# Performance work log

Hardware: AMD Instinct MI355X
Metric: run time of the kernel (lower is better)

The kernel has to match this reference:

```python
import jax, jax.numpy as jnp
import numpy as np

B, S, D, H, DH = 2, 2048, 1024, 16, 64  # batch, seq, d_hidden, n_head, d_head


def setup_inputs() -> dict:
    key = jax.random.key(0)
    ks = jax.random.split(key, 11)
    sc = 0.02
    inp = {
        "Q": jax.random.normal(ks[0], (B, S, D), jnp.float32),
        "K": jax.random.normal(ks[1], (B, S, D), jnp.float32),
        "V": jax.random.normal(ks[2], (B, S, D), jnp.float32),
        # causal mask: True = masked (strictly upper triangular), broadcast to [B,S,S]
        "attn_mask": jnp.broadcast_to(jnp.triu(jnp.ones((S, S), bool), k=1), (B, S, S)),
        "W_q": jax.random.normal(ks[3], (H * DH, D), jnp.float32) * sc,
        "b_q": jnp.zeros((H * DH,), jnp.float32),
        "W_k": jax.random.normal(ks[4], (H * DH, D), jnp.float32) * sc,
        "b_k": jnp.zeros((H * DH,), jnp.float32),
        "W_v": jax.random.normal(ks[5], (H * DH, D), jnp.float32) * sc,
        "b_v": jnp.zeros((H * DH,), jnp.float32),
        "W_o": jax.random.normal(ks[6], (D, H * DH), jnp.float32) * sc,
        "b_o": jnp.zeros((D,), jnp.float32),
    }
    return inp


def reference(Q, K, V, attn_mask, W_q, b_q, W_k, b_k, W_v, b_v, W_o, b_o):
    scaler = 1.0 / (DH ** 0.5)
    # projections: torch Linear is x @ W.T + b
    def proj(x, W, b):
        y = jnp.einsum('bsd,ed->bse', x, W) + b  # e = H*DH
        return y.reshape(x.shape[0], x.shape[1], H, DH).transpose(0, 2, 1, 3)  # [B,H,S,DH]
    q = proj(Q, W_q, b_q)
    k = proj(K, W_k, b_k)
    v = proj(V, W_v, b_v)
    score = jnp.einsum('bhqd,bhkd->bhqk', q, k) * scaler
    score = jnp.where(attn_mask[:, None, :, :], jnp.float32(-1e9), score)
    attn_prob = jax.nn.softmax(score, axis=-1)  # dropout p=0.0 -> identity
    context = jnp.einsum('bhqk,bhkd->bhqd', attn_prob, v)
    context = context.transpose(0, 2, 1, 3).reshape(Q.shape[0], -1, H * DH)
    output = jnp.einsum('bse,de->bsd', context, W_o) + b_o
    return (output, attn_prob)
```

## Files before the change

### kernel.cpp

```cpp
#include <hip/hip_runtime.h>
#include <hip/hip_bf16.h>

typedef __attribute__((ext_vector_type(8))) __bf16 bf16x8;
typedef __attribute__((ext_vector_type(4))) float f32x4;
typedef __attribute__((ext_vector_type(4))) float f4;

#define MB 2
#define MS 2048
#define MD 1024
#define MH 16
#define MDH 64

__device__ __forceinline__ void gl_lds16(const __bf16* g, __bf16* l) {
  __builtin_amdgcn_global_load_lds(
      (const __attribute__((address_space(1))) unsigned int*)g,
      (__attribute__((address_space(3))) unsigned int*)l, 16, 0, 0);
}

__device__ __forceinline__ void stage64(const __bf16* __restrict__ g, int gstride,
                                        __bf16* lds, int t) {
#pragma unroll
  for (int j = 0; j < 2; j++) {
    const int slot = t + j * 256;
    const int r = slot >> 3;
    const int c = (slot & 7) ^ (r & 7);
    gl_lds16(g + (size_t)r * gstride + c * 8, &lds[slot * 8]);
  }
}

__device__ __forceinline__ bf16x8 frag_ld(const __bf16* lds, int row, int kc) {
  const int slot = row * 8 + (kc ^ (row & 7));
  return *(const bf16x8*)&lds[slot * 8];
}

__global__ __launch_bounds__(256) void convert_kernel(
    const float* __restrict__ Q, const float* __restrict__ K, const float* __restrict__ V,
    const float* __restrict__ Wq, const float* __restrict__ Wk, const float* __restrict__ Wv,
    const float* __restrict__ Wo, __bf16* __restrict__ Ab, __bf16* __restrict__ Wb) {
  const size_t base = ((size_t)blockIdx.x * 256 + threadIdx.x) * 8;
  const float* src;
  __bf16* dst;
  size_t off;
  if (base < 3UL * 4194304UL) {
    const int z = (int)(base >> 22);
    off = base & 4194303UL;
    src = (z == 0) ? Q : ((z == 1) ? K : V);
    dst = Ab + ((size_t)z << 22);
  } else {
    const size_t b2 = base - 3UL * 4194304UL;
    const int w = (int)(b2 >> 20);
    off = b2 & 1048575UL;
    src = (w == 0) ? Wq : ((w == 1) ? Wk : ((w == 2) ? Wv : Wo));
    dst = Wb + ((size_t)w << 20);
  }
  f4 a = *(const f4*)(src + off);
  f4 b = *(const f4*)(src + off + 4);
  bf16x8 o;
#pragma unroll
  for (int j = 0; j < 4; j++) {
    o[j] = (__bf16)a[j];
    o[j + 4] = (__bf16)b[j];
  }
  *(bf16x8*)(dst + off) = o;
}

__device__ __forceinline__ void gemm_core(const __bf16* __restrict__ A,
                                          const __bf16* __restrict__ W,
                                          int tile_m, int tile_n,
                                          f32x4 acc[4][4]) {
  __shared__ __bf16 a_lds[8192];
  __shared__ __bf16 w_lds[8192];
  const int t = threadIdx.x;
  const int lane = t & 63, wave = t >> 6;
  const int l15 = lane & 15, quad = lane >> 4;
  const int wr = wave >> 1, wc = wave & 1;

  const f32x4 fzero = {0.f, 0.f, 0.f, 0.f};
#pragma unroll
  for (int mi = 0; mi < 4; mi++)
#pragma unroll
    for (int ni = 0; ni < 4; ni++) acc[mi][ni] = fzero;

  const __bf16* Abase = A + (size_t)(tile_m * 128) * 1024;
  const __bf16* Wbase = W + (size_t)(tile_n * 128) * 1024;

  for (int k0 = 0; k0 < 1024; k0 += 64) {
    __syncthreads();
#pragma unroll
    for (int j = 0; j < 4; j++) {
      const int slot = t + j * 256;
      const int r = slot >> 3;
      const int c = (slot & 7) ^ (r & 7);
      gl_lds16(Abase + (size_t)r * 1024 + k0 + c * 8, &a_lds[slot * 8]);
    }
#pragma unroll
    for (int j = 0; j < 4; j++) {
      const int slot = t + j * 256;
      const int r = slot >> 3;
      const int c = (slot & 7) ^ (r & 7);
      gl_lds16(Wbase + (size_t)r * 1024 + k0 + c * 8, &w_lds[slot * 8]);
    }
    __syncthreads();

#pragma unroll
    for (int kk = 0; kk < 2; kk++) {
      bf16x8 af[4], bf[4];
#pragma unroll
      for (int mi = 0; mi < 4; mi++)
        af[mi] = frag_ld(a_lds, wr * 64 + mi * 16 + l15, kk * 4 + quad);
#pragma unroll
      for (int ni = 0; ni < 4; ni++)
        bf[ni] = frag_ld(w_lds, wc * 64 + ni * 16 + l15, kk * 4 + quad);
#pragma unroll
      for (int mi = 0; mi < 4; mi++)
#pragma unroll
        for (int ni = 0; ni < 4; ni++)
          acc[mi][ni] = __builtin_amdgcn_mfma_f32_16x16x32_bf16(af[mi], bf[ni], acc[mi][ni], 0, 0, 0);
    }
  }
}

__global__ __launch_bounds__(256) void qkv_proj(
    const __bf16* __restrict__ Ab, const __bf16* __restrict__ Wb,
    const float* __restrict__ bq, const float* __restrict__ bk, const float* __restrict__ bv,
    __bf16* __restrict__ qo, __bf16* __restrict__ ko, __bf16* __restrict__ vo) {
  const int z = blockIdx.z;
  const __bf16* A = Ab + ((size_t)z << 22);
  const __bf16* W = Wb + ((size_t)z << 20);
  const float* bias = (z == 0) ? bq : ((z == 1) ? bk : bv);
  __bf16* out = (z == 0) ? qo : ((z == 1) ? ko : vo);

  f32x4 acc[4][4];
  gemm_core(A, W, blockIdx.y, blockIdx.x, acc);

  const int t = threadIdx.x;
  const int lane = t & 63, wave = t >> 6;
  const int l15 = lane & 15, quad = lane >> 4;
  const int wr = wave >> 1, wc = wave & 1;
  const float scale = (z == 0) ? 0.125f : 1.0f;

#pragma unroll
  for (int ni = 0; ni < 4; ni++) {
    const int e = blockIdx.x * 128 + wc * 64 + ni * 16 + l15;
    const float bias_v = bias[e];
    const int h = e >> 6, dh = e & 63;
#pragma unroll
    for (int mi = 0; mi < 4; mi++) {
#pragma unroll
      for (int r = 0; r < 4; r++) {
        const int sg = blockIdx.y * 128 + wr * 64 + mi * 16 + quad * 4 + r;
        const int bb = sg >> 11, s = sg & 2047;
        const float val = (acc[mi][ni][r] + bias_v) * scale;
        size_t addr;
        if (z < 2) addr = ((size_t)((bb * 16 + h) * 2048 + s)) * 64 + dh;
        else       addr = ((size_t)((bb * 16 + h) * 64 + dh)) * 2048 + s;
        out[addr] = (__bf16)val;
      }
    }
  }
}

__device__ __forceinline__ void qk_tile(const __bf16* kl, const bf16x8 qf0, const bf16x8 qf1,
                                        int l15, int quad, f32x4 sc[4]) {
  const f32x4 fzero = {0.f, 0.f, 0.f, 0.f};
#pragma unroll
  for (int blk = 0; blk < 4; blk++) {
    bf16x8 kf0 = frag_ld(kl, blk * 16 + l15, quad);
    bf16x8 kf1 = frag_ld(kl, blk * 16 + l15, 4 + quad);
    f32x4 z = fzero;
    z = __builtin_amdgcn_mfma_f32_16x16x32_bf16(qf0, kf0, z, 0, 0, 0);
    z = __builtin_amdgcn_mfma_f32_16x16x32_bf16(qf1, kf1, z, 0, 0, 0);
    sc[blk] = z;
  }
}

__device__ __forceinline__ void sm_update(const f32x4 sc[4], int kt, int q0, int wave,
                                          int quad, int l15, float m[4], float l[4]) {
#pragma unroll
  for (int r = 0; r < 4; r++) {
    const int qrow = q0 + wave * 16 + quad * 4 + r;
    float sv[4];
    float nm = m[r];
#pragma unroll
    for (int blk = 0; blk < 4; blk++) {
      const int kcol = kt * 64 + blk * 16 + l15;
      float s = sc[blk][r];
      s = (kcol > qrow) ? -1e30f : s;
      sv[blk] = s;
      nm = fmaxf(nm, s);
    }
    float acc = l[r] * __expf(m[r] - nm);
#pragma unroll
    for (int blk = 0; blk < 4; blk++) acc += __expf(sv[blk] - nm);
    l[r] = acc;
    m[r] = nm;
  }
}

__global__ __launch_bounds__(256) void attn_kernel(
    const __bf16* __restrict__ q, const __bf16* __restrict__ k,
    const __bf16* __restrict__ vt, float* __restrict__ P, __bf16* __restrict__ ctx) {
  const int qt = 31 - blockIdx.x;
  const int h = blockIdx.y, b = blockIdx.z;
  const int bh = b * 16 + h;
  const int t = threadIdx.x;
  const int lane = t & 63, wave = t >> 6;
  const int l15 = lane & 15, quad = lane >> 4;
  const int q0 = qt * 64;

  __shared__ __bf16 q_lds[4096];
  __shared__ __bf16 k_lds[4096];
  __shared__ __bf16 v_lds[4096];
  __shared__ __bf16 p_lds[4 * 16 * 72];

  const __bf16* qbase = q + ((size_t)bh * 2048 + q0) * 64;
  const __bf16* kbase = k + (size_t)bh * 2048 * 64;
  const __bf16* vbase = vt + (size_t)bh * 64 * 2048;
  float* Pbase = P + ((size_t)bh * 2048 + q0) * 2048;

  stage64(qbase, 64, q_lds, t);
  __syncthreads();
  const bf16x8 qf0 = frag_ld(q_lds, wave * 16 + l15, quad);
  const bf16x8 qf1 = frag_ld(q_lds, wave * 16 + l15, 4 + quad);

  float m[4], l[4];
#pragma unroll
  for (int r = 0; r < 4; r++) { m[r] = -1e30f; l[r] = 0.f; }

  for (int kt0 = 0; kt0 <= qt; kt0 += 2) {
    const bool two = (kt0 + 1 <= qt);
    __syncthreads();
    stage64(kbase + (size_t)kt0 * 4096, 64, k_lds, t);
    if (two) stage64(kbase + (size_t)(kt0 + 1) * 4096, 64, v_lds, t);
    __syncthreads();
    f32x4 sc[4];
    qk_tile(k_lds, qf0, qf1, l15, quad, sc);
    sm_update(sc, kt0, q0, wave, quad, l15, m, l);
    if (two) {
      qk_tile(v_lds, qf0, qf1, l15, quad, sc);
      sm_update(sc, kt0 + 1, q0, wave, quad, l15, m, l);
    }
  }

  float rl[4];
#pragma unroll
  for (int r = 0; r < 4; r++) {
    float mm = m[r], ll = l[r];
#pragma unroll
    for (int msk = 1; msk < 16; msk <<= 1) {
      const float mo = __shfl_xor(mm, msk, 64);
      const float lo = __shfl_xor(ll, msk, 64);
      const float mn = fmaxf(mm, mo);
      ll = ll * __expf(mm - mn) + lo * __expf(mo - mn);
      mm = mn;
    }
    m[r] = mm;
    rl[r] = 1.0f / ll;
  }

  const f32x4 fzero = {0.f, 0.f, 0.f, 0.f};
  f32x4 o[4];
#pragma unroll
  for (int d = 0; d < 4; d++) o[d] = fzero;

  for (int kt = 0; kt <= qt; kt++) {
    __syncthreads();
    stage64(kbase + (size_t)kt * 4096, 64, k_lds, t);
    stage64(vbase + (size_t)kt * 64, 2048, v_lds, t);
    __syncthreads();

    f32x4 sc[4];
    qk_tile(k_lds, qf0, qf1, l15, quad, sc);

#pragma unroll
    for (int r = 0; r < 4; r++) {
      const int qrow = q0 + wave * 16 + quad * 4 + r;
#pragma unroll
      for (int blk = 0; blk < 4; blk++) {
        const int kcol = kt * 64 + blk * 16 + l15;
        float s = sc[blk][r];
        s = (kcol > qrow) ? -1e30f : s;
        const float p = __expf(s - m[r]) * rl[r];
        Pbase[(size_t)(wave * 16 + quad * 4 + r) * 2048 + kcol] = p;
        p_lds[(wave * 16 + quad * 4 + r) * 72 + blk * 16 + l15] = (__bf16)p;
      }
    }
    const bf16x8 pf0 = *(const bf16x8*)&p_lds[(wave * 16 + l15) * 72 + quad * 8];
    const bf16x8 pf1 = *(const bf16x8*)&p_lds[(wave * 16 + l15) * 72 + 32 + quad * 8];
#pragma unroll
    for (int d = 0; d < 4; d++) {
      bf16x8 vf0 = frag_ld(v_lds, d * 16 + l15, quad);
      bf16x8 vf1 = frag_ld(v_lds, d * 16 + l15, 4 + quad);
      o[d] = __builtin_amdgcn_mfma_f32_16x16x32_bf16(pf0, vf0, o[d], 0, 0, 0);
      o[d] = __builtin_amdgcn_mfma_f32_16x16x32_bf16(pf1, vf1, o[d], 0, 0, 0);
    }
  }

  const int c0 = (qt + 1) * 64;
  const int zr = t >> 2;
  for (int c = c0 + (t & 3) * 4; c < 2048; c += 16)
    *(f32x4*)&Pbase[(size_t)zr * 2048 + c] = fzero;

#pragma unroll
  for (int d = 0; d < 4; d++) {
#pragma unroll
    for (int r = 0; r < 4; r++) {
      const int sl = wave * 16 + quad * 4 + r;
      const size_t idx = ((size_t)(b * 2048 + q0 + sl)) * 1024 + h * 64 + d * 16 + l15;
      ctx[idx] = (__bf16)o[d][r];
    }
  }
}

__global__ __launch_bounds__(256) void out_proj(
    const __bf16* __restrict__ ctxp, const __bf16* __restrict__ Wob,
    const float* __restrict__ bo, float* __restrict__ out) {
  f32x4 acc[4][4];
  gemm_core(ctxp, Wob, blockIdx.y, blockIdx.x, acc);

  const int t = threadIdx.x;
  const int lane = t & 63, wave = t >> 6;
  const int l15 = lane & 15, quad = lane >> 4;
  const int wr = wave >> 1, wc = wave & 1;

#pragma unroll
  for (int ni = 0; ni < 4; ni++) {
    const int e = blockIdx.x * 128 + wc * 64 + ni * 16 + l15;
    const float bias_v = bo[e];
#pragma unroll
    for (int mi = 0; mi < 4; mi++) {
#pragma unroll
      for (int r = 0; r < 4; r++) {
        const int sg = blockIdx.y * 128 + wr * 64 + mi * 16 + quad * 4 + r;
        out[(size_t)sg * 1024 + e] = acc[mi][ni][r] + bias_v;
      }
    }
  }
}

extern "C" void kernel_launch(void* const* d_in, const int* in_sizes, int n_in,
                              void* d_out, int out_size, void* d_ws, size_t ws_size,
                              hipStream_t stream) {
  const float* Q  = (const float*)d_in[0];
  const float* K  = (const float*)d_in[1];
  const float* V  = (const float*)d_in[2];
  const float* Wq = (const float*)d_in[4];
  const float* bq = (const float*)d_in[5];
  const float* Wk = (const float*)d_in[6];
  const float* bk = (const float*)d_in[7];
  const float* Wv = (const float*)d_in[8];
  const float* bv = (const float*)d_in[9];
  const float* Wo = (const float*)d_in[10];
  const float* bo = (const float*)d_in[11];

  float* out0 = (float*)d_out;
  float* P = out0 + (size_t)MB * MS * MD;

  __bf16* Ab  = (__bf16*)d_ws;
  __bf16* Wb  = Ab + 3UL * 4194304UL;
  __bf16* qws = Wb + 4UL * 1048576UL;
  __bf16* kws = qws + 4194304UL;
  __bf16* vws = kws + 4194304UL;
  __bf16* cws = vws + 4194304UL;

  convert_kernel<<<dim3(8192), 256, 0, stream>>>(Q, K, V, Wq, Wk, Wv, Wo, Ab, Wb);
  qkv_proj<<<dim3(8, 32, 3), 256, 0, stream>>>(Ab, Wb, bq, bk, bv, qws, kws, vws);
  attn_kernel<<<dim3(32, 16, 2), 256, 0, stream>>>(qws, kws, vws, P, cws);
  out_proj<<<dim3(8, 32, 1), 256, 0, stream>>>(cws, Wb + 3UL * 1048576UL, bo, out0);
}
```

Before: 772.4 us.

## Double-buffer K/V staging, swizzle P LDS, remap blocks, and specialize diagonal masking

Both attention passes now prefetch the next K (and V) tiles into alternate LDS buffers while computing on the current ones. This cuts one barrier per iteration and overlaps global-to-LDS loads with MFMA work. The P staging buffer uses an XOR swizzle in place of padding to avoid bank conflicts. Causal masking is applied only on the diagonal tile. Blocks are remapped so consecutive blocks span different heads at the same q-tile, and s_setprio raises priority around the MFMA sections. The cost is more LDS (5 tiles) and more complex indexing.

```diff
diff --git a/kernel.cpp b/kernel.cpp
--- a/kernel.cpp
+++ b/kernel.cpp
@@ -175,7 +175,8 @@
 }
 
 __device__ __forceinline__ void sm_update(const f32x4 sc[4], int kt, int q0, int wave,
-                                          int quad, int l15, float m[4], float l[4]) {
+                                          int quad, int l15, float m[4], float l[4],
+                                          bool diag) {
 #pragma unroll
   for (int r = 0; r < 4; r++) {
     const int qrow = q0 + wave * 16 + quad * 4 + r;
@@ -185,7 +186,7 @@
     for (int blk = 0; blk < 4; blk++) {
       const int kcol = kt * 64 + blk * 16 + l15;
       float s = sc[blk][r];
-      s = (kcol > qrow) ? -1e30f : s;
+      if (diag) s = (kcol > qrow) ? -1e30f : s;
       sv[blk] = s;
       nm = fmaxf(nm, s);
     }
@@ -197,49 +198,83 @@
   }
 }
 
+__device__ __forceinline__ void p_emit(const f32x4 sc[4], bool diag, int kt, int q0,
+                                       int wave, int quad, int l15,
+                                       const float m[4], const float rl[4],
+                                       float* __restrict__ Pbase, __bf16* p_lds) {
+#pragma unroll
+  for (int r = 0; r < 4; r++) {
+    const int rr = quad * 4 + r;
+    const int qrow = q0 + wave * 16 + rr;
+#pragma unroll
+    for (int blk = 0; blk < 4; blk++) {
+      const int kcol = kt * 64 + blk * 16 + l15;
+      float s = sc[blk][r];
+      if (diag) s = (kcol > qrow) ? -1e30f : s;
+      const float p = __expf(s - m[r]) * rl[r];
+      Pbase[(size_t)(wave * 16 + rr) * 2048 + kcol] = p;
+      const int cc = blk * 16 + l15;
+      const int sch = (cc >> 3) ^ (rr & 7);
+      p_lds[wave * 1024 + rr * 64 + sch * 8 + (cc & 7)] = (__bf16)p;
+    }
+  }
+}
+
 __global__ __launch_bounds__(256) void attn_kernel(
     const __bf16* __restrict__ q, const __bf16* __restrict__ k,
     const __bf16* __restrict__ vt, float* __restrict__ P, __bf16* __restrict__ ctx) {
-  const int qt = 31 - blockIdx.x;
-  const int h = blockIdx.y, b = blockIdx.z;
-  const int bh = b * 16 + h;
+  const int lin = blockIdx.x + 32 * (blockIdx.y + 16 * blockIdx.z);
+  const int x8 = lin & 7, j = lin >> 3;
+  const int bh = x8 + 8 * (j & 3);
+  const int qt = 31 - (j >> 2);
+  const int b = bh >> 4, h = bh & 15;
   const int t = threadIdx.x;
   const int lane = t & 63, wave = t >> 6;
   const int l15 = lane & 15, quad = lane >> 4;
   const int q0 = qt * 64;
 
-  __shared__ __bf16 q_lds[4096];
-  __shared__ __bf16 k_lds[4096];
-  __shared__ __bf16 v_lds[4096];
-  __shared__ __bf16 p_lds[4 * 16 * 72];
+  __shared__ __bf16 sbuf[4][4096];
+  __shared__ __bf16 p_lds[4096];
 
   const __bf16* qbase = q + ((size_t)bh * 2048 + q0) * 64;
   const __bf16* kbase = k + (size_t)bh * 2048 * 64;
   const __bf16* vbase = vt + (size_t)bh * 64 * 2048;
   float* Pbase = P + ((size_t)bh * 2048 + q0) * 2048;
 
-  stage64(qbase, 64, q_lds, t);
+  stage64(qbase, 64, sbuf[0], t);
   __syncthreads();
-  const bf16x8 qf0 = frag_ld(q_lds, wave * 16 + l15, quad);
-  const bf16x8 qf1 = frag_ld(q_lds, wave * 16 + l15, 4 + quad);
+  const bf16x8 qf0 = frag_ld(sbuf[0], wave * 16 + l15, quad);
+  const bf16x8 qf1 = frag_ld(sbuf[0], wave * 16 + l15, 4 + quad);
+  __syncthreads();
 
   float m[4], l[4];
 #pragma unroll
   for (int r = 0; r < 4; r++) { m[r] = -1e30f; l[r] = 0.f; }
 
+  stage64(kbase, 64, sbuf[0], t);
+  if (qt >= 1) stage64(kbase + 4096, 64, sbuf[1], t);
+  __syncthreads();
   for (int kt0 = 0; kt0 <= qt; kt0 += 2) {
-    const bool two = (kt0 + 1 <= qt);
+    const int pb = (kt0 & 2);
+    const int nx = kt0 + 2;
+    if (nx <= qt) {
+      stage64(kbase + (size_t)nx * 4096, 64, sbuf[2 - pb], t);
+      if (nx + 1 <= qt) stage64(kbase + (size_t)(nx + 1) * 4096, 64, sbuf[3 - pb], t);
+    }
+    f32x4 sc[4];
+    __builtin_amdgcn_s_setprio(1);
+    qk_tile(sbuf[pb], qf0, qf1, l15, quad, sc);
+    __builtin_amdgcn_s_setprio(0);
+    if (kt0 == qt) sm_update(sc, kt0, q0, wave, quad, l15, m, l, true);
+    else           sm_update(sc, kt0, q0, wave, quad, l15, m, l, false);
+    if (kt0 + 1 <= qt) {
+      __builtin_amdgcn_s_setprio(1);
+      qk_tile(sbuf[pb + 1], qf0, qf1, l15, quad, sc);
+      __builtin_amdgcn_s_setprio(0);
+      if (kt0 + 1 == qt) sm_update(sc, kt0 + 1, q0, wave, quad, l15, m, l, true);
+      else               sm_update(sc, kt0 + 1, q0, wave, quad, l15, m, l, false);
+    }
     __syncthreads();
-    stage64(kbase + (size_t)kt0 * 4096, 64, k_lds, t);
-    if (two) stage64(kbase + (size_t)(kt0 + 1) * 4096, 64, v_lds, t);
-    __syncthreads();
-    f32x4 sc[4];
-    qk_tile(k_lds, qf0, qf1, l15, quad, sc);
-    sm_update(sc, kt0, q0, wave, quad, l15, m, l);
-    if (two) {
-      qk_tile(v_lds, qf0, qf1, l15, quad, sc);
-      sm_update(sc, kt0 + 1, q0, wave, quad, l15, m, l);
-    }
   }
 
   float rl[4];
@@ -263,37 +298,35 @@
 #pragma unroll
   for (int d = 0; d < 4; d++) o[d] = fzero;
 
+  stage64(kbase, 64, sbuf[0], t);
+  stage64(vbase, 2048, sbuf[2], t);
+  __syncthreads();
   for (int kt = 0; kt <= qt; kt++) {
-    __syncthreads();
-    stage64(kbase + (size_t)kt * 4096, 64, k_lds, t);
-    stage64(vbase + (size_t)kt * 64, 2048, v_lds, t);
-    __syncthreads();
-
+    const int cb = kt & 1;
+    if (kt < qt) {
+      stage64(kbase + (size_t)(kt + 1) * 4096, 64, sbuf[cb ^ 1], t);
+      stage64(vbase + (size_t)(kt + 1) * 64, 2048, sbuf[2 + (cb ^ 1)], t);
+    }
     f32x4 sc[4];
-    qk_tile(k_lds, qf0, qf1, l15, quad, sc);
-
-#pragma unroll
-    for (int r = 0; r < 4; r++) {
-      const int qrow = q0 + wave * 16 + quad * 4 + r;
-#pragma unroll
-      for (int blk = 0; blk < 4; blk++) {
-        const int kcol = kt * 64 + blk * 16 + l15;
-        float s = sc[blk][r];
-        s = (kcol > qrow) ? -1e30f : s;
-        const float p = __expf(s - m[r]) * rl[r];
-        Pbase[(size_t)(wave * 16 + quad * 4 + r) * 2048 + kcol] = p;
-        p_lds[(wave * 16 + quad * 4 + r) * 72 + blk * 16 + l15] = (__bf16)p;
-      }
-    }
-    const bf16x8 pf0 = *(const bf16x8*)&p_lds[(wave * 16 + l15) * 72 + quad * 8];
-    const bf16x8 pf1 = *(const bf16x8*)&p_lds[(wave * 16 + l15) * 72 + 32 + quad * 8];
+    __builtin_amdgcn_s_setprio(1);
+    qk_tile(sbuf[cb], qf0, qf1, l15, quad, sc);
+    __builtin_amdgcn_s_setprio(0);
+
+    if (kt == qt) p_emit(sc, true, kt, q0, wave, quad, l15, m, rl, Pbase, p_lds);
+    else          p_emit(sc, false, kt, q0, wave, quad, l15, m, rl, Pbase, p_lds);
+
+    const bf16x8 pf0 = *(const bf16x8*)&p_lds[wave * 1024 + l15 * 64 + ((quad ^ (l15 & 7)) << 3)];
+    const bf16x8 pf1 = *(const bf16x8*)&p_lds[wave * 1024 + l15 * 64 + (((4 + quad) ^ (l15 & 7)) << 3)];
+    __builtin_amdgcn_s_setprio(1);
 #pragma unroll
     for (int d = 0; d < 4; d++) {
-      bf16x8 vf0 = frag_ld(v_lds, d * 16 + l15, quad);
-      bf16x8 vf1 = frag_ld(v_lds, d * 16 + l15, 4 + quad);
+      bf16x8 vf0 = frag_ld(sbuf[2 + cb], d * 16 + l15, quad);
+      bf16x8 vf1 = frag_ld(sbuf[2 + cb], d * 16 + l15, 4 + quad);
       o[d] = __builtin_amdgcn_mfma_f32_16x16x32_bf16(pf0, vf0, o[d], 0, 0, 0);
       o[d] = __builtin_amdgcn_mfma_f32_16x16x32_bf16(pf1, vf1, o[d], 0, 0, 0);
     }
+    __builtin_amdgcn_s_setprio(0);
+    __syncthreads();
   }
 
   const int c0 = (qt + 1) * 64;
```

After: 773.0 us. Within noise of the previous version (+0.1%).
